# Kernel optimization log

Measured on AMD Instinct MI355X. Metric: run time of the kernel, lower is better.

The kernel has to match this reference:

```python
import jax, jax.numpy as jnp
import numpy as np

C = 256          # in_channels == inter_channels (structurally required)
B, H, W = 16, 64, 64


def setup_inputs() -> dict:
    key = jax.random.key(0)
    ks = jax.random.split(key, 10)
    s = 1.0 / np.sqrt(C)
    x = jax.random.normal(ks[0], (B, C, H, W), dtype=jnp.float32)
    # theta / phi: 1x1 convs, stored as [out, in]
    theta_w = jax.random.normal(ks[1], (C, C), dtype=jnp.float32) * s
    theta_b = jax.random.normal(ks[2], (C,), dtype=jnp.float32) * s
    phi_w = jax.random.normal(ks[3], (C, C), dtype=jnp.float32) * s
    phi_b = jax.random.normal(ks[4], (C,), dtype=jnp.float32) * s
    # grouped conv: Conv2d(C, 2C, kernel=(C,1), groups=C).
    # torch weight [2C, 1, C, 1] with group-major out-channel order -> [C groups, 2 per group, C taps]
    gw = jax.random.normal(ks[5], (C, 2, C), dtype=jnp.float32) * s
    gb = jax.random.normal(ks[6], (C, 2), dtype=jnp.float32) * s
    # dim_adjust: 1x1 conv 2C -> C, stored as [C, 2C]
    dw = jax.random.normal(ks[7], (C, 2 * C), dtype=jnp.float32) * (1.0 / np.sqrt(2 * C))
    db = jax.random.normal(ks[8], (C,), dtype=jnp.float32) * (1.0 / np.sqrt(2 * C))
    return {"x": x, "theta_w": theta_w, "theta_b": theta_b,
            "phi_w": phi_w, "phi_b": phi_b,
            "gw": gw, "gb": gb, "dw": dw, "db": db}


def reference(x, theta_w, theta_b, phi_w, phi_b, gw, gb, dw, db):
    b, c, h, w = x.shape
    xf = x.reshape(b, c, h * w)                                   # [B,C,HW]
    theta = jnp.einsum('oc,bcn->bon', theta_w, xf) + theta_b[:, None]  # [B,Ci,HW]
    phi = jnp.einsum('oc,bcn->bon', phi_w, xf) + phi_b[:, None]        # [B,Ci,HW]
    f = jnp.einsum('bon,bpn->bop', theta, phi)                    # [B,Ci,Ci] channel similarity
    # grouped conv: group g sees channel g of f over its 'spatial' axis (length Ci),
    # producing 2 outputs per group via a full-height dot product.
    g = jnp.einsum('bgk,gjk->bgj', f, gw) + gb                    # [B,C,2]
    g = jax.nn.relu(g).reshape(b, 2 * c)                          # [B,2C]
    out = jnp.einsum('bo,co->bc', g, dw) + db                     # [B,C] 1x1 conv
    return out[:, :, None, None]                                  # [B,C,1,1]
```

## Files before the change

kernel.cpp:

```cpp
#include <hip/hip_runtime.h>


#define CC  256
#define NB  16
#define HWN 4096
#define KSPLIT 16
#define NPAIR 136

typedef __attribute__((ext_vector_type(4))) float f32x4;
typedef __attribute__((ext_vector_type(8))) short bf16x8;

__device__ inline unsigned short f2bf(float f) {
  unsigned u = __float_as_uint(f);
  u += 0x7fff + ((u >> 16) & 1);
  return (unsigned short)(u >> 16);
}
__device__ inline float bf2f(unsigned u) { return __uint_as_float(u << 16); }

__global__ __launch_bounds__(1024, 4) void k_gram(const float* __restrict__ x,
                                                  unsigned short* __restrict__ slab,
                                                  float* __restrict__ Spart) {
  __shared__ __align__(16) unsigned short As[2][256 * 64];
  const int blk = blockIdx.x, tid = threadIdx.x;
  const int ks = blk >> 4, b = blk & 15;
  const float* xb = x + (size_t)b * CC * HWN;

  const int w = tid >> 6, lane = tid & 63;
  const int quad = lane >> 4, m15 = lane & 15;
  const int srow = tid >> 4;
  const int scol = (tid & 15) << 2;
  const int sg = scol >> 3, so = scol & 7;

  f32x4 acc[16];
  #pragma unroll
  for (int i = 0; i < 16; ++i) acc[i] = (f32x4){0.f, 0.f, 0.f, 0.f};
  float rs[4] = {0.f, 0.f, 0.f, 0.f};

  const int k0 = ks * 256;
  float4 ld[4];
  #pragma unroll
  for (int p = 0; p < 4; ++p)
    ld[p] = *(const float4*)(xb + (size_t)(p * 64 + srow) * HWN + k0 + scol);
  #pragma unroll
  for (int p = 0; p < 4; ++p) {
    const int row = p * 64 + srow;
    rs[p] += ld[p].x + ld[p].y + ld[p].z + ld[p].w;
    *(ushort4*)&As[0][row * 64 + ((sg ^ (row & 7)) << 3) + so] =
        make_ushort4(f2bf(ld[p].x), f2bf(ld[p].y), f2bf(ld[p].z), f2bf(ld[p].w));
  }
  __syncthreads();

  #pragma unroll
  for (int i = 0; i < 4; ++i) {
    const int cur = i & 1;
    if (i < 3) {
      const int kc = k0 + (i + 1) * 64;
      #pragma unroll
      for (int p = 0; p < 4; ++p)
        ld[p] = *(const float4*)(xb + (size_t)(p * 64 + srow) * HWN + kc + scol);
    }
    const int rowa = 16 * w + m15;
    #pragma unroll
    for (int kkg = 0; kkg < 8; kkg += 4) {
      const int ga = (kkg + quad) ^ (m15 & 7);
      bf16x8 af = *(const bf16x8*)&As[cur][rowa * 64 + ga * 8];
      #pragma unroll
      for (int ct = 0; ct < 16; ++ct) {
        if (ct < w) continue;
        bf16x8 bfr = *(const bf16x8*)&As[cur][(16 * ct + m15) * 64 + ga * 8];
        acc[ct] = __builtin_amdgcn_mfma_f32_16x16x32_bf16(af, bfr, acc[ct], 0, 0, 0);
      }
    }
    if (i < 3) {
      #pragma unroll
      for (int p = 0; p < 4; ++p) {
        const int row = p * 64 + srow;
        rs[p] += ld[p].x + ld[p].y + ld[p].z + ld[p].w;
        *(ushort4*)&As[1 - cur][row * 64 + ((sg ^ (row & 7)) << 3) + so] =
            make_ushort4(f2bf(ld[p].x), f2bf(ld[p].y), f2bf(ld[p].z), f2bf(ld[p].w));
      }
    }
    __syncthreads();
  }

  const int off_w = 16 * w - (w * (w - 1)) / 2;
  unsigned short* sbase = slab + ((size_t)(ks * 16 + b) * NPAIR) * 256;
  #pragma unroll
  for (int ct = 0; ct < 16; ++ct) {
    if (ct < w) continue;
    const int pid = off_w + (ct - w);
    uint2 ov;
    ov.x = (unsigned)f2bf(acc[ct][0]) | ((unsigned)f2bf(acc[ct][1]) << 16);
    ov.y = (unsigned)f2bf(acc[ct][2]) | ((unsigned)f2bf(acc[ct][3]) << 16);
    *(uint2*)(sbase + pid * 256 + lane * 4) = ov;
  }

  #pragma unroll
  for (int p = 0; p < 4; ++p) {
    float v = rs[p];
    v += __shfl_xor(v, 1);
    v += __shfl_xor(v, 2);
    v += __shfl_xor(v, 4);
    v += __shfl_xor(v, 8);
    if ((tid & 15) == 0)
      Spart[(ks * 16 + b) * 256 + p * 64 + srow] = v;
  }
}

__global__ __launch_bounds__(256) void k_fuse2(const unsigned short* __restrict__ slab,
                                               const float* __restrict__ Spart,
                                               const float* __restrict__ gw,
                                               const float* __restrict__ pw,
                                               const float* __restrict__ pb,
                                               const float* __restrict__ tw,
                                               const float* __restrict__ db,
                                               unsigned short* __restrict__ Gh,
                                               unsigned short* __restrict__ Qh,
                                               float* __restrict__ E,
                                               float* __restrict__ U,
                                               float* __restrict__ V,
                                               float* __restrict__ out) {
  const int blk = blockIdx.x, tid = threadIdx.x;
  if (blk < 544) {
    const int t = blk * 256 + tid;
    const int b = t / 8704;
    const int rem = t % 8704;
    const int pid0 = rem >> 6, lane = rem & 63;
    int w = 0, p = pid0;
    while (p >= 16 - w) { p -= 16 - w; ++w; }
    const int ct = w + p;
    const int quad = lane >> 4, m15 = lane & 15;
    float s[4] = {0.f, 0.f, 0.f, 0.f};
    const unsigned short* sp = slab + (size_t)(b * NPAIR + pid0) * 256 + lane * 4;
    #pragma unroll
    for (int ks = 0; ks < KSPLIT; ++ks) {
      const uint2 v = *(const uint2*)(sp + (size_t)ks * 16 * NPAIR * 256);
      s[0] += bf2f(v.x & 0xffffu); s[1] += bf2f(v.x >> 16);
      s[2] += bf2f(v.y & 0xffffu); s[3] += bf2f(v.y >> 16);
    }
    unsigned short h[4];
    #pragma unroll
    for (int r = 0; r < 4; ++r) h[r] = f2bf(s[r]);
    unsigned short* Gb = Gh + ((size_t)b << 16);
    const int rb = 16 * w + quad * 4;
    const int col = 16 * ct + m15;
    #pragma unroll
    for (int r = 0; r < 4; ++r) Gb[(rb + r) * 256 + col] = h[r];
    uint2 mv;
    mv.x = (unsigned)h[0] | ((unsigned)h[1] << 16);
    mv.y = (unsigned)h[2] | ((unsigned)h[3] << 16);
    *(uint2*)(Gb + col * 256 + rb) = mv;
  } else if (blk < 1056) {
    const int rj = blk - 544;
    __shared__ float smg[260];
    smg[tid] = gw[rj * 256 + tid];
    __syncthreads();
    float q0 = 0.f, q1 = 0.f, q2 = 0.f, q3 = 0.f;
    #pragma unroll 4
    for (int o = 0; o < 256; o += 4) {
      q0 += smg[o]     * pw[o * 256 + tid];
      q1 += smg[o + 1] * pw[(o + 1) * 256 + tid];
      q2 += smg[o + 2] * pw[(o + 2) * 256 + tid];
      q3 += smg[o + 3] * pw[(o + 3) * 256 + tid];
    }
    Qh[rj * 256 + tid] = f2bf((q0 + q1) + (q2 + q3));
    float e = smg[tid] * pb[tid];
    e += __shfl_xor(e, 1);
    e += __shfl_xor(e, 2);
    e += __shfl_xor(e, 4);
    e += __shfl_xor(e, 8);
    e += __shfl_xor(e, 16);
    e += __shfl_xor(e, 32);
    if ((tid & 63) == 0) smg[256 + (tid >> 6)] = e;
    __syncthreads();
    if (tid == 0) E[rj] = smg[256] + smg[257] + smg[258] + smg[259];
  } else if (blk < 1088) {
    const int m = blk - 1056;
    const int b = m & 15, mat = m >> 4;
    const float* Wm = mat ? pw : tw;
    float* outp = mat ? V : U;
    __shared__ float sm[256];
    float sv = 0.f;
    #pragma unroll
    for (int ks = 0; ks < KSPLIT; ++ks)
      sv += Spart[(ks * 16 + b) * 256 + tid];
    sm[tid] = sv;
    __syncthreads();
    const int l = tid & 15, oh = tid >> 4;
    #pragma unroll
    for (int oc = 0; oc < 16; ++oc) {
      const int o = oc * 16 + oh;
      float a = 0.f;
      #pragma unroll
      for (int j = 0; j < 16; ++j)
        a += Wm[o * 256 + l * 16 + j] * sm[l * 16 + j];
      a += __shfl_xor(a, 1);
      a += __shfl_xor(a, 2);
      a += __shfl_xor(a, 4);
      a += __shfl_xor(a, 8);
      if (l == 0) outp[b * 256 + o] = a;
    }
  } else {
    const int b = blk - 1088;
    out[b * 256 + tid] = db[tid];
  }
}

__global__ __launch_bounds__(256) void k_p(const unsigned short* __restrict__ Gh,
                                           const unsigned short* __restrict__ Qh,
                                           const float* __restrict__ tw,
                                           const float* __restrict__ gw,
                                           const float* __restrict__ U,
                                           const float* __restrict__ V,
                                           const float* __restrict__ E,
                                           const float* __restrict__ tb,
                                           const float* __restrict__ gb,
                                           const float* __restrict__ dw,
                                           float* __restrict__ out) {
  const int rjt = blockIdx.x, b = blockIdx.y;
  const int rj0 = rjt * 16;
  const int tid = threadIdx.x, w = tid >> 6, lane = tid & 63;
  const int quad = lane >> 4, m15 = lane & 15;
  const unsigned short* Gb = Gh + ((size_t)b << 16);

  f32x4 acc[4];
  #pragma unroll
  for (int mt = 0; mt < 4; ++mt) acc[mt] = (f32x4){0.f, 0.f, 0.f, 0.f};

  #pragma unroll
  for (int s = 0; s < 8; ++s) {
    const int kb = s * 32 + quad * 8;
    bf16x8 bq = *(const bf16x8*)(Qh + (rj0 + m15) * 256 + kb);
    #pragma unroll
    for (int mt = 0; mt < 4; ++mt) {
      bf16x8 ag = *(const bf16x8*)(Gb + (64 * w + 16 * mt + m15) * 256 + kb);
      acc[mt] = __builtin_amdgcn_mfma_f32_16x16x32_bf16(ag, bq, acc[mt], 0, 0, 0);
    }
  }

  __shared__ float sred[16 * 4];
  __shared__ float sred2[16];
  __shared__ float gsh[16];
  {
    const int rj = rj0 + m15;
    const int r = rj >> 1;
    float p = 0.f;
    #pragma unroll
    for (int mt = 0; mt < 4; ++mt)
      #pragma unroll
      for (int reg = 0; reg < 4; ++reg)
        p += acc[mt][reg] * tw[r * 256 + 64 * w + 16 * mt + quad * 4 + reg];
    p += __shfl_xor(p, 16);
    p += __shfl_xor(p, 32);
    if (quad == 0) sred[m15 * 4 + w] = p;
  }
  {
    const int oi = tid >> 4, seg = tid & 15;
    const int rj = rj0 + oi;
    float p2 = 0.f;
    #pragma unroll
    for (int i = 0; i < 16; ++i) {
      const int cp = seg * 16 + i;
      p2 += gw[rj * 256 + cp] * V[b * 256 + cp];
    }
    p2 += __shfl_xor(p2, 1);
    p2 += __shfl_xor(p2, 2);
    p2 += __shfl_xor(p2, 4);
    p2 += __shfl_xor(p2, 8);
    if (seg == 0) sred2[oi] = p2;
  }
  __syncthreads();
  if (tid < 16) {
    const int rj = rj0 + tid, r = rj >> 1;
    const float v = sred[tid * 4] + sred[tid * 4 + 1] +
                    sred[tid * 4 + 2] + sred[tid * 4 + 3];
    const float tbr = tb[r];
    const float bias = tbr * sred2[tid] +
                       (U[b * 256 + r] + 4096.0f * tbr) * E[rj] + gb[rj];
    gsh[tid] = fmaxf(v + bias, 0.f);
  }
  __syncthreads();
  float a = 0.f;
  #pragma unroll
  for (int i = 0; i < 16; ++i)
    a += gsh[i] * dw[tid * 512 + rj0 + i];
  atomicAdd(&out[b * 256 + tid], a);
}

extern "C" void kernel_launch(void* const* d_in, const int* in_sizes, int n_in,
                              void* d_out, int out_size, void* d_ws, size_t ws_size,
                              hipStream_t stream) {
  const float* x  = (const float*)d_in[0];
  const float* tw = (const float*)d_in[1];
  const float* tb = (const float*)d_in[2];
  const float* pw = (const float*)d_in[3];
  const float* pb = (const float*)d_in[4];
  const float* gw = (const float*)d_in[5];
  const float* gb = (const float*)d_in[6];
  const float* dw = (const float*)d_in[7];
  const float* db = (const float*)d_in[8];
  float* out = (float*)d_out;

  unsigned short* slab = (unsigned short*)d_ws;
  unsigned short* Gh   = slab + (size_t)KSPLIT * 16 * NPAIR * 256;
  unsigned short* Qh   = Gh + ((size_t)16 << 16);
  float* Spart = (float*)(Qh + 512 * 256);
  float* E  = Spart + KSPLIT * 16 * 256;
  float* U  = E + 512;
  float* V  = U + NB * 256;

  k_gram<<<256, 1024, 0, stream>>>(x, slab, Spart);
  k_fuse2<<<1104, 256, 0, stream>>>(slab, Spart, gw, pw, pb, tw, db,
                                    Gh, Qh, E, U, V, out);
  k_p<<<dim3(32, NB), 256, 0, stream>>>(Gh, Qh, tw, gw, U, V, E, tb, gb, dw, out);
}
```

Measured before the change: 147.6 us.

## Split Gram kernel blocks into two row-halves with 512 threads each

The channel-Gram kernel changes from 256 blocks of 1024 threads to 512 blocks of 512 threads. Each (k-split, batch) tile is now shared by two blocks. The first block computes the upper-triangle tiles for rows 0-127 and loads all 256 channels. The second block computes the 128x128 lower-right triangle and loads only the upper 128 channels. The aim is more, smaller blocks for better occupancy and scheduling. The cost is extra reads of x (the first half re-reads rows 128-255) and uneven work between the two halves.

```diff
diff --git a/kernel.cpp b/kernel.cpp
--- a/kernel.cpp
+++ b/kernel.cpp
@@ -17,12 +17,13 @@
 }
 __device__ inline float bf2f(unsigned u) { return __uint_as_float(u << 16); }
 
-__global__ __launch_bounds__(1024, 4) void k_gram(const float* __restrict__ x,
-                                                  unsigned short* __restrict__ slab,
-                                                  float* __restrict__ Spart) {
+__global__ __launch_bounds__(512, 4) void k_gram(const float* __restrict__ x,
+                                                 unsigned short* __restrict__ slab,
+                                                 float* __restrict__ Spart) {
   __shared__ __align__(16) unsigned short As[2][256 * 64];
   const int blk = blockIdx.x, tid = threadIdx.x;
-  const int ks = blk >> 4, b = blk & 15;
+  const int half = blk >> 8;
+  const int ks = (blk >> 4) & 15, b = blk & 15;
   const float* xb = x + (size_t)b * CC * HWN;
 
   const int w = tid >> 6, lane = tid & 63;
@@ -30,34 +31,46 @@
   const int srow = tid >> 4;
   const int scol = (tid & 15) << 2;
   const int sg = scol >> 3, so = scol & 7;
+  const int grow0 = half ? 128 : 0;
+  const int k0 = ks * 256;
 
   f32x4 acc[16];
   #pragma unroll
   for (int i = 0; i < 16; ++i) acc[i] = (f32x4){0.f, 0.f, 0.f, 0.f};
   float rs[4] = {0.f, 0.f, 0.f, 0.f};
 
-  const int k0 = ks * 256;
   float4 ld[4];
   #pragma unroll
   for (int p = 0; p < 4; ++p)
-    ld[p] = *(const float4*)(xb + (size_t)(p * 64 + srow) * HWN + k0 + scol);
+    ld[p] = *(const float4*)(xb + (size_t)(grow0 + p * 32 + srow) * HWN + k0 + scol);
   #pragma unroll
   for (int p = 0; p < 4; ++p) {
-    const int row = p * 64 + srow;
+    const int lrow = p * 32 + srow;
     rs[p] += ld[p].x + ld[p].y + ld[p].z + ld[p].w;
-    *(ushort4*)&As[0][row * 64 + ((sg ^ (row & 7)) << 3) + so] =
+    *(ushort4*)&As[0][lrow * 64 + ((sg ^ (lrow & 7)) << 3) + so] =
         make_ushort4(f2bf(ld[p].x), f2bf(ld[p].y), f2bf(ld[p].z), f2bf(ld[p].w));
+  }
+  if (!half) {
+    #pragma unroll
+    for (int p = 0; p < 4; ++p)
+      ld[p] = *(const float4*)(xb + (size_t)(128 + p * 32 + srow) * HWN + k0 + scol);
+    #pragma unroll
+    for (int p = 0; p < 4; ++p) {
+      const int lrow = 128 + p * 32 + srow;
+      *(ushort4*)&As[0][lrow * 64 + ((sg ^ (lrow & 7)) << 3) + so] =
+          make_ushort4(f2bf(ld[p].x), f2bf(ld[p].y), f2bf(ld[p].z), f2bf(ld[p].w));
+    }
   }
   __syncthreads();
 
   #pragma unroll
   for (int i = 0; i < 4; ++i) {
     const int cur = i & 1;
+    const int kc = k0 + (i + 1) * 64;
     if (i < 3) {
-      const int kc = k0 + (i + 1) * 64;
       #pragma unroll
       for (int p = 0; p < 4; ++p)
-        ld[p] = *(const float4*)(xb + (size_t)(p * 64 + srow) * HWN + kc + scol);
+        ld[p] = *(const float4*)(xb + (size_t)(grow0 + p * 32 + srow) * HWN + kc + scol);
     }
     const int rowa = 16 * w + m15;
     #pragma unroll
@@ -67,6 +80,7 @@
       #pragma unroll
       for (int ct = 0; ct < 16; ++ct) {
         if (ct < w) continue;
+        if (half && ct >= 8) continue;
         bf16x8 bfr = *(const bf16x8*)&As[cur][(16 * ct + m15) * 64 + ga * 8];
         acc[ct] = __builtin_amdgcn_mfma_f32_16x16x32_bf16(af, bfr, acc[ct], 0, 0, 0);
       }
@@ -74,21 +88,34 @@
     if (i < 3) {
       #pragma unroll
       for (int p = 0; p < 4; ++p) {
-        const int row = p * 64 + srow;
+        const int lrow = p * 32 + srow;
         rs[p] += ld[p].x + ld[p].y + ld[p].z + ld[p].w;
-        *(ushort4*)&As[1 - cur][row * 64 + ((sg ^ (row & 7)) << 3) + so] =
+        *(ushort4*)&As[1 - cur][lrow * 64 + ((sg ^ (lrow & 7)) << 3) + so] =
             make_ushort4(f2bf(ld[p].x), f2bf(ld[p].y), f2bf(ld[p].z), f2bf(ld[p].w));
       }
+      if (!half) {
+        #pragma unroll
+        for (int p = 0; p < 4; ++p)
+          ld[p] = *(const float4*)(xb + (size_t)(128 + p * 32 + srow) * HWN + kc + scol);
+        #pragma unroll
+        for (int p = 0; p < 4; ++p) {
+          const int lrow = 128 + p * 32 + srow;
+          *(ushort4*)&As[1 - cur][lrow * 64 + ((sg ^ (lrow & 7)) << 3) + so] =
+              make_ushort4(f2bf(ld[p].x), f2bf(ld[p].y), f2bf(ld[p].z), f2bf(ld[p].w));
+        }
+      }
     }
     __syncthreads();
   }
 
-  const int off_w = 16 * w - (w * (w - 1)) / 2;
+  const int Wt = half * 8 + w;
+  const int off = 16 * Wt - (Wt * (Wt - 1)) / 2;
   unsigned short* sbase = slab + ((size_t)(ks * 16 + b) * NPAIR) * 256;
   #pragma unroll
   for (int ct = 0; ct < 16; ++ct) {
     if (ct < w) continue;
-    const int pid = off_w + (ct - w);
+    if (half && ct >= 8) continue;
+    const int pid = off + (ct - w);
     uint2 ov;
     ov.x = (unsigned)f2bf(acc[ct][0]) | ((unsigned)f2bf(acc[ct][1]) << 16);
     ov.y = (unsigned)f2bf(acc[ct][2]) | ((unsigned)f2bf(acc[ct][3]) << 16);
@@ -103,7 +130,7 @@
     v += __shfl_xor(v, 4);
     v += __shfl_xor(v, 8);
     if ((tid & 15) == 0)
-      Spart[(ks * 16 + b) * 256 + p * 64 + srow] = v;
+      Spart[(ks * 16 + b) * 256 + grow0 + p * 32 + srow] = v;
   }
 }
 
@@ -309,7 +336,7 @@
   float* U  = E + 512;
   float* V  = U + NB * 256;
 
-  k_gram<<<256, 1024, 0, stream>>>(x, slab, Spart);
+  k_gram<<<512, 512, 0, stream>>>(x, slab, Spart);
   k_fuse2<<<1104, 256, 0, stream>>>(slab, Spart, gw, pw, pb, tw, db,
                                     Gh, Qh, E, U, V, out);
   k_p<<<dim3(32, NB), 256, 0, stream>>>(Gh, Qh, tw, gw, U, V, E, tb, gb, dw, out);
```

Measured after the change: 155.9 us. +5.7%, slower.
